# Kernel tuning notes

Hardware: AMD Instinct MI355X
Metric: run time of the kernel (lower is better)

The kernel has to match this reference:

```python
import jax, jax.numpy as jnp
import numpy as np

# Qwen3.5 GatedDeltaNet dims
B, T, HID = 2, 2048, 2048
HK, HV, DK, DV, KW = 16, 32, 128, 128, 4   # k-heads, v-heads, head dims, conv kernel
R = HV // HK                                # GQA repeat factor = 2
KEY_DIM = HK * DK                           # 2048
VAL_DIM = HV * DV                           # 4096
CONV_DIM = 2 * KEY_DIM + VAL_DIM            # 8192
EPS = 1e-6


def setup_inputs() -> dict:
    key = jax.random.key(0)
    ks = jax.random.split(key, 10)
    w = lambda k, shape, s=0.02: (jax.random.normal(k, shape) * s).astype(jnp.float32)
    A = jax.random.uniform(ks[8], (HV,), minval=1e-3, maxval=16.0)
    return {
        "hidden_states": jax.random.normal(ks[0], (B, T, HID), jnp.float32),
        "W_qkv": w(ks[1], (HID, CONV_DIM)),
        "W_z": w(ks[2], (HID, VAL_DIM)),
        "W_b": w(ks[3], (HID, HV)),
        "W_a": w(ks[4], (HID, HV)),
        "conv_w": w(ks[5], (CONV_DIM, KW), 0.5),   # depthwise causal conv taps
        "dt_bias": jnp.ones((HV,), jnp.float32),
        "A_log": jnp.log(A).astype(jnp.float32),
        "norm_weight": jnp.ones((DV,), jnp.float32),
        "W_out": w(ks[9], (VAL_DIM, HID)),
    }


def _forward(hidden_states, W_qkv, W_z, W_b, W_a, conv_w, dt_bias, A_log, norm_weight, W_out):
    x = hidden_states
    # --- projections ---
    qkv = x @ W_qkv                                    # [B,T,CONV_DIM]
    z = x @ W_z                                        # [B,T,VAL_DIM]
    beta = jax.nn.sigmoid(x @ W_b)                     # [B,T,HV]
    alpha = x @ W_a                                    # [B,T,HV]
    g = -jnp.exp(A_log) * jax.nn.softplus(alpha + dt_bias)  # [B,T,HV] (log-decay <= 0)

    # --- fix_query_key_value_ordering: per-k-head interleaved layout ---
    qkv = qkv.reshape(B, T, HK, 2 * DK + R * DV)
    q, k, v = jnp.split(qkv, [DK, 2 * DK], axis=3)
    mixed = jnp.concatenate([q.reshape(B, T, -1), k.reshape(B, T, -1), v.reshape(B, T, -1)], axis=-1)

    # --- causal depthwise short conv (kernel 4) + SiLU ---
    xp = jnp.pad(mixed, ((0, 0), (KW - 1, 0), (0, 0)))
    conv = sum(conv_w[:, i] * xp[:, i:i + T, :] for i in range(KW))
    conv = jax.nn.silu(conv)

    q, k, v = jnp.split(conv, [KEY_DIM, 2 * KEY_DIM], axis=-1)
    q = q.reshape(B, T, HK, DK)
    k = k.reshape(B, T, HK, DK)
    v = v.reshape(B, T, HV, DV)
    gate = z.reshape(B, T, HV, DV)

    # GQA: repeat q,k heads to match v heads
    q = jnp.repeat(q, R, axis=2)                       # [B,T,HV,DK]
    k = jnp.repeat(k, R, axis=2)

    # l2-norm q,k (use_qk_l2norm_in_kernel=True) and default scale 1/sqrt(DK)
    q = q / jnp.sqrt(jnp.sum(q * q, axis=-1, keepdims=True) + 1e-6)
    k = k / jnp.sqrt(jnp.sum(k * k, axis=-1, keepdims=True) + 1e-6)
    q = q * (DK ** -0.5)

    # --- gated delta rule recurrence (scan over time) ---
    # state S: [B,HV,DK,DV];  S_t = a_t*S_{t-1} + k_t (beta_t*(v_t - (a_t*S_{t-1})^T k_t))^T
    def step(S, inp):
        qt, kt, vt, gt, bt = inp                       # [B,HV,DK],[B,HV,DK],[B,HV,DV],[B,HV],[B,HV]
        S = S * jnp.exp(gt)[:, :, None, None]
        kv = jnp.einsum('bhk,bhkv->bhv', kt, S)
        delta = bt[..., None] * (vt - kv)              # [B,HV,DV]
        S = S + kt[..., None] * delta[:, :, None, :]
        o = jnp.einsum('bhk,bhkv->bhv', qt, S)
        return S, o

    tfirst = lambda a: jnp.moveaxis(a, 1, 0)           # [T,B,...]
    S0 = jnp.zeros((B, HV, DK, DV), q.dtype)
    _, o = jax.lax.scan(step, S0, (tfirst(q), tfirst(k), tfirst(v), tfirst(g), tfirst(beta)))
    o = jnp.moveaxis(o, 0, 1)                          # [B,T,HV,DV]

    # --- gated RMSNorm: rmsnorm(o) * silu(gate) * weight ---
    var = jnp.mean(o * o, axis=-1, keepdims=True)
    o = o * jax.lax.rsqrt(var + EPS)
    o = o * jax.nn.silu(gate)
    o = o * norm_weight

    return o.reshape(B, T, VAL_DIM) @ W_out            # [B,T,HID]


def reference(hidden_states, W_qkv, W_z, W_b, W_a, conv_w, dt_bias, A_log, norm_weight, W_out):
    return _forward(hidden_states, W_qkv, W_z, W_b, W_a, conv_w, dt_bias, A_log, norm_weight, W_out)
```

## Files before the change

### kernel.cpp

```cpp
#include <hip/hip_runtime.h>


#define T_LEN 2048
#define MROWS 4096

typedef __bf16 bf16x8 __attribute__((ext_vector_type(8)));
typedef float f32x4 __attribute__((ext_vector_type(4)));

#define MFMA(a, b, c) __builtin_amdgcn_mfma_f32_16x16x32_bf16((a), (b), (c), 0, 0, 0)

__device__ __forceinline__ unsigned short f2bf(float f) {
  unsigned int u = __float_as_uint(f);
  unsigned int r = (u + 0x7fffu + ((u >> 16) & 1u)) >> 16;
  return (unsigned short)r;
}
__device__ __forceinline__ float bf2f(unsigned short u) {
  return __uint_as_float(((unsigned int)u) << 16);
}
__device__ __forceinline__ void gload_lds16(const void* g, void* l) {
  __builtin_amdgcn_global_load_lds(
      (const __attribute__((address_space(1))) unsigned int*)g,
      (__attribute__((address_space(3))) unsigned int*)l, 16, 0, 0);
}

__global__ __launch_bounds__(256) void f32_to_bf16_vec(const float* __restrict__ src,
                                                       unsigned short* __restrict__ dst,
                                                       int n4) {
  int i = blockIdx.x * 256 + threadIdx.x;
  if (i >= n4) return;
  float4 v = ((const float4*)src)[i];
  ushort4 o;
  o.x = f2bf(v.x); o.y = f2bf(v.y); o.z = f2bf(v.z); o.w = f2bf(v.w);
  ((ushort4*)dst)[i] = o;
}

__global__ __launch_bounds__(256) void transpose_f2b(const float* __restrict__ src,
                                                     unsigned short* __restrict__ dst,
                                                     int R, int C) {
  __shared__ float tile[32][33];
  int tx = threadIdx.x & 31, ty = threadIdx.x >> 5;
  int c0 = blockIdx.x * 32, r0 = blockIdx.y * 32;
  #pragma unroll
  for (int i = ty; i < 32; i += 8)
    tile[i][tx] = src[(size_t)(r0 + i) * C + c0 + tx];
  __syncthreads();
  #pragma unroll
  for (int i = ty; i < 32; i += 8)
    dst[(size_t)(c0 + i) * R + r0 + tx] = f2bf(tile[tx][i]);
}

template <int OUTBF>
__global__ __launch_bounds__(512, 2) void gemm8p(const unsigned short* __restrict__ A, int lda,
                                                 const unsigned short* __restrict__ Bt, int ldb,
                                                 void* __restrict__ Cv, int ldc,
                                                 int M, int N, int K) {
  __shared__ unsigned short lds[65536];

  const int mtiles = M >> 8;
  const int nwg = gridDim.x, orig = blockIdx.x;
  const int q = nwg >> 3, r = nwg & 7;
  const int xcd = orig & 7, idx = orig >> 3;
  const int swz = (xcd < r ? xcd * (q + 1) : r * (q + 1) + (xcd - r) * q) + idx;
  const int m0 = (swz % mtiles) * 256;
  const int n0 = (swz / mtiles) * 256;

  const int tid = threadIdx.x, lane = tid & 63, wv = tid >> 6;
  const int wm = wv >> 2, wn = wv & 3;
  const int l15 = lane & 15, l4 = lane >> 4;

  f32x4 acc[8][4];
  #pragma unroll
  for (int i = 0; i < 8; i++)
    #pragma unroll
    for (int j = 0; j < 4; j++) acc[i][j] = f32x4{0.f, 0.f, 0.f, 0.f};

  const int NT = K >> 6;

  auto SHALF = [&](int t, int op, int h) {
    unsigned short* base = lds + (t & 1) * 32768 + op * 16384 + h * 8192;
    const unsigned short* G = op ? Bt : A;
    const int ld = op ? ldb : lda;
    const int r0g = (op ? n0 : m0) + h * 128;
    const int k0 = t << 6;
    #pragma unroll
    for (int is = 0; is < 2; is++) {
      int ow = is * 8192 + wv * 1024;
      int o = ow + lane * 16;
      int row = o >> 7, colB = o & 127;
      int scol = colB ^ ((row & 7) << 4);
      gload_lds16(G + (size_t)(r0g + row) * ld + k0 + (scol >> 1), base + (ow >> 1));
    }
  };

  bf16x8 aF[4][2], bF[2][2];
  auto RD_A = [&](int t, int qm) {
    const unsigned short* base = lds + (t & 1) * 32768 + qm * 8192;
    #pragma unroll
    for (int mi = 0; mi < 4; mi++) {
      int ra = wm * 64 + mi * 16 + l15;
      int sw = (ra & 7) << 4;
      #pragma unroll
      for (int kh = 0; kh < 2; kh++) {
        int colB = kh * 64 + l4 * 16;
        aF[mi][kh] = *(const bf16x8*)(base + ra * 64 + ((colB ^ sw) >> 1));
      }
    }
  };
  auto RD_B = [&](int t, int qn) {
    const unsigned short* base = lds + (t & 1) * 32768 + 16384 + qn * 8192;
    #pragma unroll
    for (int ni = 0; ni < 2; ni++) {
      int rb = wn * 32 + ni * 16 + l15;
      int sw = (rb & 7) << 4;
      #pragma unroll
      for (int kh = 0; kh < 2; kh++) {
        int colB = kh * 64 + l4 * 16;
        bF[ni][kh] = *(const bf16x8*)(base + rb * 64 + ((colB ^ sw) >> 1));
      }
    }
  };
  auto COMPUTE = [&](int qm, int qn) {
    __builtin_amdgcn_s_setprio(1);
    #pragma unroll
    for (int mi = 0; mi < 4; mi++)
      #pragma unroll
      for (int ni = 0; ni < 2; ni++)
        #pragma unroll
        for (int kh = 0; kh < 2; kh++)
          acc[qm * 4 + mi][qn * 2 + ni] =
              MFMA(aF[mi][kh], bF[ni][kh], acc[qm * 4 + mi][qn * 2 + ni]);
    __builtin_amdgcn_s_setprio(0);
  };
  auto SBAR = [&]() {
    __builtin_amdgcn_sched_barrier(0);
    __builtin_amdgcn_s_barrier();
    __builtin_amdgcn_sched_barrier(0);
  };

  SHALF(0, 0, 0); SHALF(0, 1, 0); SHALF(0, 1, 1); SHALF(0, 0, 1);
  asm volatile("s_waitcnt vmcnt(4)" ::: "memory");
  SBAR();

  for (int t = 0; t < NT; t++) {
    const bool lastT = (t + 1 >= NT);
    RD_A(t, 0); RD_B(t, 0);
    if (!lastT) SHALF(t + 1, 0, 0);
    COMPUTE(0, 0);
    if (!lastT) asm volatile("s_waitcnt vmcnt(4)" ::: "memory");
    else        asm volatile("s_waitcnt vmcnt(2)" ::: "memory");
    SBAR();
    RD_B(t, 1);
    if (!lastT) SHALF(t + 1, 1, 0);
    COMPUTE(0, 1);
    if (!lastT) asm volatile("s_waitcnt vmcnt(4)" ::: "memory");
    else        asm volatile("s_waitcnt vmcnt(0)" ::: "memory");
    SBAR();
    RD_A(t, 1);
    if (!lastT) SHALF(t + 1, 1, 1);
    COMPUTE(1, 1);
    RD_B(t, 0);
    if (!lastT) SHALF(t + 1, 0, 1);
    COMPUTE(1, 0);
    if (!lastT) {
      asm volatile("s_waitcnt vmcnt(4)" ::: "memory");
      SBAR();
    }
  }

  #pragma unroll
  for (int i = 0; i < 8; i++) {
    int grow = m0 + (i >> 2) * 128 + wm * 64 + (i & 3) * 16 + l4 * 4;
    #pragma unroll
    for (int j = 0; j < 4; j++) {
      int gcol = n0 + (j >> 1) * 128 + wn * 32 + (j & 1) * 16 + l15;
      if (OUTBF) {
        unsigned short* cp = (unsigned short*)Cv + (size_t)grow * ldc + gcol;
        #pragma unroll
        for (int rr = 0; rr < 4; rr++) cp[(size_t)rr * ldc] = f2bf(acc[i][j][rr]);
      } else {
        float* cp = (float*)Cv + (size_t)grow * ldc + gcol;
        #pragma unroll
        for (int rr = 0; rr < 4; rr++) cp[(size_t)rr * ldc] = acc[i][j][rr];
      }
    }
  }
}

template <int OUTBF, int BN>
__global__ __launch_bounds__(512, 2) void gemm256(const unsigned short* __restrict__ A, int lda,
                                                  const unsigned short* __restrict__ Bt, int ldb,
                                                  void* __restrict__ Cv, int ldc,
                                                  int M, int N, int K) {
  constexpr int BUFSZ = 16384 + BN * 64;
  constexpr int BISS = BN / 64;
  constexpr int IS = 4 + BISS;
  constexpr int WMv = (BN == 256) ? 2 : 4;
  constexpr int MSUB = 256 / (WMv * 16);
  constexpr int MSPAN = 256 / WMv;

  __shared__ unsigned short lds[2 * BUFSZ];

  const int mtiles = M >> 8;
  const int nwg = gridDim.x;
  const int orig = blockIdx.x;
  const int q = nwg >> 3, r = nwg & 7;
  const int xcd = orig & 7, idx = orig >> 3;
  const int swz = (xcd < r ? xcd * (q + 1) : r * (q + 1) + (xcd - r) * q) + idx;
  const int m0 = (swz % mtiles) * 256;
  const int n0 = (swz / mtiles) * BN;

  const int tid = threadIdx.x, lane = tid & 63, wv = tid >> 6;
  const int wm = (BN == 256) ? (wv >> 2) : (wv >> 1);
  const int wn = (BN == 256) ? (wv & 3) : (wv & 1);
  const int l15 = lane & 15, l4 = lane >> 4;

  f32x4 acc[MSUB][4];
  #pragma unroll
  for (int i = 0; i < MSUB; i++)
    #pragma unroll
    for (int j = 0; j < 4; j++) acc[i][j] = f32x4{0.f, 0.f, 0.f, 0.f};

  const int NT = K >> 6;

  auto STAGE = [&](int kt) {
    unsigned short* base = lds + (kt & 1) * BUFSZ;
    const int k0 = kt << 6;
    #pragma unroll
    for (int is = 0; is < 4; is++) {
      int ow = is * 8192 + wv * 1024;
      int o = ow + lane * 16;
      int row = o >> 7, colB = o & 127;
      int scol = colB ^ ((row & 7) << 4);
      gload_lds16(A + (size_t)(m0 + row) * lda + k0 + (scol >> 1), base + (ow >> 1));
    }
    #pragma unroll
    for (int is = 0; is < BISS; is++) {
      int ow = is * 8192 + wv * 1024;
      int o = ow + lane * 16;
      int row = o >> 7, colB = o & 127;
      int scol = colB ^ ((row & 7) << 4);
      gload_lds16(Bt + (size_t)(n0 + row) * ldb + k0 + (scol >> 1), base + 16384 + (ow >> 1));
    }
  };

  STAGE(0);
  if (NT > 1) STAGE(1);
  if constexpr (IS == 8) asm volatile("s_waitcnt vmcnt(8)" ::: "memory");
  else                   asm volatile("s_waitcnt vmcnt(6)" ::: "memory");
  __builtin_amdgcn_sched_barrier(0);
  __builtin_amdgcn_s_barrier();
  __builtin_amdgcn_sched_barrier(0);

  for (int t = 0; t < NT; t++) {
    const unsigned short* Abuf = lds + (t & 1) * BUFSZ;
    const unsigned short* Bbuf = Abuf + 16384;
    bf16x8 bF[4][2];
    #pragma unroll
    for (int n = 0; n < 4; n++) {
      int rb = wn * 64 + n * 16 + l15;
      int sw = (rb & 7) << 4;
      #pragma unroll
      for (int ks = 0; ks < 2; ks++) {
        int colB = (ks * 32 + l4 * 8) * 2;
        bF[n][ks] = *(const bf16x8*)(Bbuf + rb * 64 + ((colB ^ sw) >> 1));
      }
    }
    __builtin_amdgcn_s_setprio(1);
    #pragma unroll
    for (int m = 0; m < MSUB; m++) {
      int ra = wm * MSPAN + m * 16 + l15;
      int sw = (ra & 7) << 4;
      int c0b = l4 * 16;
      bf16x8 a0 = *(const bf16x8*)(Abuf + ra * 64 + ((c0b ^ sw) >> 1));
      bf16x8 a1 = *(const bf16x8*)(Abuf + ra * 64 + (((64 + c0b) ^ sw) >> 1));
      #pragma unroll
      for (int n = 0; n < 4; n++) {
        acc[m][n] = MFMA(a0, bF[n][0], acc[m][n]);
        acc[m][n] = MFMA(a1, bF[n][1], acc[m][n]);
      }
    }
    __builtin_amdgcn_s_setprio(0);
    __builtin_amdgcn_sched_barrier(0);
    __builtin_amdgcn_s_barrier();
    __builtin_amdgcn_sched_barrier(0);
    if (t + 2 < NT) STAGE(t + 2);
    if (t + 1 < NT) {
      if (t + 2 < NT) {
        if constexpr (IS == 8) asm volatile("s_waitcnt vmcnt(8)" ::: "memory");
        else                   asm volatile("s_waitcnt vmcnt(6)" ::: "memory");
      } else {
        asm volatile("s_waitcnt vmcnt(0)" ::: "memory");
      }
      __builtin_amdgcn_sched_barrier(0);
      __builtin_amdgcn_s_barrier();
      __builtin_amdgcn_sched_barrier(0);
    }
  }

  #pragma unroll
  for (int m = 0; m < MSUB; m++) {
    int grow = m0 + wm * MSPAN + m * 16 + l4 * 4;
    #pragma unroll
    for (int n = 0; n < 4; n++) {
      int gcol = n0 + wn * 64 + n * 16 + l15;
      if (OUTBF) {
        unsigned short* cp = (unsigned short*)Cv + (size_t)grow * ldc + gcol;
        #pragma unroll
        for (int rr = 0; rr < 4; rr++) cp[(size_t)rr * ldc] = f2bf(acc[m][n][rr]);
      } else {
        float* cp = (float*)Cv + (size_t)grow * ldc + gcol;
        #pragma unroll
        for (int rr = 0; rr < 4; rr++) cp[(size_t)rr * ldc] = acc[m][n][rr];
      }
    }
  }
}

template <int OUTBF>
__global__ __launch_bounds__(256) void gemm_bf16(const unsigned short* __restrict__ A, int lda,
                                                 const unsigned short* __restrict__ Bt, int ldb,
                                                 void* __restrict__ Cv, int ldc,
                                                 int M, int N, int K) {
  __shared__ unsigned short As[128 * 64];
  __shared__ unsigned short Bs[128 * 64];
  const int tid = threadIdx.x, lane = tid & 63, wv = tid >> 6;
  const int wr = wv >> 1, wc = wv & 1;
  const int m0 = blockIdx.y * 128, n0 = blockIdx.x * 128;
  const int lrow8 = lane >> 3;
  const int lk8 = (lane & 7) * 8;

  f32x4 acc[4][4];
  #pragma unroll
  for (int i = 0; i < 4; i++)
    #pragma unroll
    for (int j = 0; j < 4; j++) acc[i][j] = f32x4{0.f, 0.f, 0.f, 0.f};

  for (int k0 = 0; k0 < K; k0 += 64) {
    #pragma unroll
    for (int j = 0; j < 4; ++j) {
      int chunk = j * 4 + wv;
      int r = chunk * 8 + lrow8;
      gload_lds16(A + (size_t)(m0 + r) * lda + k0 + lk8, (void*)(As + chunk * 512));
      gload_lds16(Bt + (size_t)(n0 + r) * ldb + k0 + lk8, (void*)(Bs + chunk * 512));
    }
    __syncthreads();
    #pragma unroll
    for (int half = 0; half < 2; ++half) {
      int ko = half * 32 + (lane >> 4) * 8;
      bf16x8 af[4], bfr[4];
      #pragma unroll
      for (int i = 0; i < 4; i++) {
        int ra = wr * 64 + i * 16 + (lane & 15);
        af[i] = *(const bf16x8*)(As + ra * 64 + ko);
        int rb = wc * 64 + i * 16 + (lane & 15);
        bfr[i] = *(const bf16x8*)(Bs + rb * 64 + ko);
      }
      #pragma unroll
      for (int i = 0; i < 4; i++)
        #pragma unroll
        for (int j = 0; j < 4; j++)
          acc[i][j] = MFMA(af[i], bfr[j], acc[i][j]);
    }
    __syncthreads();
  }
  int cr4 = (lane >> 4) * 4;
  int cc = lane & 15;
  #pragma unroll
  for (int i = 0; i < 4; i++) {
    int row = m0 + wr * 64 + i * 16 + cr4;
    #pragma unroll
    for (int j = 0; j < 4; j++) {
      int col = n0 + wc * 64 + j * 16 + cc;
      if (OUTBF) {
        unsigned short* cp = (unsigned short*)Cv + (size_t)row * ldc + col;
        #pragma unroll
        for (int r = 0; r < 4; r++) cp[(size_t)r * ldc] = f2bf(acc[i][j][r]);
      } else {
        float* cp = (float*)Cv + (size_t)row * ldc + col;
        #pragma unroll
        for (int r = 0; r < 4; r++) cp[(size_t)r * ldc] = acc[i][j][r];
      }
    }
  }
}

__global__ __launch_bounds__(256) void beta_g_kernel(const unsigned short* __restrict__ ba,
                                                     const float* __restrict__ A_log,
                                                     const float* __restrict__ dt_bias,
                                                     unsigned short* __restrict__ betab,
                                                     float* __restrict__ g) {
  int i = blockIdx.x * 256 + threadIdx.x;
  int row = i >> 5, hv = i & 31;
  float rb = bf2f(ba[(size_t)row * 128 + hv]);
  float ra = bf2f(ba[(size_t)row * 128 + 32 + hv]);
  betab[i] = f2bf(1.f / (1.f + expf(-rb)));
  float xg = ra + dt_bias[hv];
  float sp = (xg > 20.f) ? xg : log1pf(expf(xg));
  g[i] = -expf(A_log[hv]) * sp;
}

__global__ __launch_bounds__(256) void conv_kernel(const unsigned short* __restrict__ qkv,
                                                   const float* __restrict__ conv_w,
                                                   unsigned short* __restrict__ out) {
  const int seg = blockIdx.x, tt = blockIdx.y, b = blockIdx.z;
  const int tid = threadIdx.x;
  const int c0 = seg * 128;
  const bool isq = seg < 16;
  int scb;
  if (isq) scb = seg * 512;
  else if (seg < 32) scb = (seg - 16) * 512 + 128;
  else scb = ((seg - 32) >> 1) * 512 + 256 + ((seg - 32) & 1) * 128;

  __shared__ unsigned short raw[35][136];
  __shared__ float cw[4][132];

  for (int i = tid; i < 512; i += 256) {
    int cl = i >> 2, tap = i & 3;
    cw[tap][cl] = conv_w[(size_t)(c0 + cl) * 4 + tap];
  }
  const int t0 = tt * 32;
  for (int i = tid; i < 560; i += 256) {
    int row = i >> 4, col = (i & 15) * 8;
    int gt = t0 - 3 + row;
    uint4 v = make_uint4(0u, 0u, 0u, 0u);
    if (gt >= 0) v = *(const uint4*)(qkv + (size_t)(b * T_LEN + gt) * 8192 + scb + col);
    *(uint4*)(&raw[row][col]) = v;
  }
  __syncthreads();
  const int s = tid >> 3, dg = tid & 7;
  union RawU { uint4 v[2]; unsigned short h[16]; };
  RawU u[4];
  #pragma unroll
  for (int i = 0; i < 4; i++) {
    const uint4* p = (const uint4*)&raw[s + i][dg * 16];
    u[i].v[0] = p[0]; u[i].v[1] = p[1];
  }
  float vals[16]; float ss = 0.f;
  #pragma unroll
  for (int j = 0; j < 16; j++) {
    float a = 0.f;
    #pragma unroll
    for (int i = 0; i < 4; i++) a = fmaf(cw[i][dg * 16 + j], bf2f(u[i].h[j]), a);
    a = a / (1.f + expf(-a));
    vals[j] = a; ss += a * a;
  }
  if (seg < 32) {
    ss += __shfl_xor(ss, 1); ss += __shfl_xor(ss, 2); ss += __shfl_xor(ss, 4);
    float sc = rsqrtf(ss + 1e-6f);
    if (isq) sc *= 0.08838834764831845f;
    #pragma unroll
    for (int j = 0; j < 16; j++) vals[j] *= sc;
  }
  union { uint4 v[2]; unsigned short h[16]; } ov;
  #pragma unroll
  for (int j = 0; j < 16; j++) ov.h[j] = f2bf(vals[j]);
  unsigned short* op = out + (size_t)(b * T_LEN + t0 + s) * 8192 + c0 + dg * 16;
  *(uint4*)(op) = ov.v[0];
  *(uint4*)(op + 8) = ov.v[1];
}

__global__ __launch_bounds__(256) void prep_kernel(const unsigned short* __restrict__ conv,
                                                   const float* __restrict__ g,
                                                   const unsigned short* __restrict__ betab,
                                                   unsigned short* __restrict__ M1g,
                                                   unsigned short* __restrict__ M2g,
                                                   unsigned char* __restrict__ vecs) {
  const int c = blockIdx.x, bh = blockIdx.y;
  const int b = bh >> 5, hv = bh & 31, hk = hv >> 1;
  const int bhc = bh * 32 + c;
  const int tid = threadIdx.x, lane = tid & 63, wv = tid >> 6;
  const int r0 = b * T_LEN + c * 64;
  const int l15 = lane & 15, l4 = lane >> 4;

  __shared__ unsigned short Kb[128 * 72];
  __shared__ unsigned short QbX[64 * 136];
  __shared__ unsigned short Lbf[64 * 72];
  __shared__ unsigned short Pb[64 * 72];
  __shared__ unsigned short WT[3 * 16 * 40];
  __shared__ float Gs[64], SCs[64], BLs[64];

  unsigned short* Qb = QbX;
  unsigned short* XTb = QbX;
  unsigned short* Xdrow = QbX + 4608;

  if (wv == 0) {
    float gt = g[(size_t)(r0 + lane) * 32 + hv];
    #pragma unroll
    for (int d = 1; d < 64; d <<= 1) {
      float o = __shfl_up(gt, (unsigned)d, 64);
      if (lane >= d) gt += o;
    }
    float GC = __shfl(gt, 63, 64);
    float lam = expf(gt);
    float beta = bf2f(betab[(size_t)(r0 + lane) * 32 + hv]);
    Gs[lane] = gt;
    SCs[lane] = expf(GC - gt);
    BLs[lane] = beta;
    unsigned short* vb16 = (unsigned short*)(vecs + (size_t)bhc * 272);
    vb16[lane] = f2bf(beta * lam);
    vb16[64 + lane] = f2bf(lam);
    if (lane == 0) *(float*)(vecs + (size_t)bhc * 272 + 256) = expf(GC);
  }
  const unsigned short* Kg = conv + (size_t)r0 * 8192 + 2048 + hk * 128;
  const unsigned short* Qg = conv + (size_t)r0 * 8192 + hk * 128;
  for (int u = tid; u < 1024; u += 256) {
    int row = u >> 4, col = (u & 15) * 8;
    *(uint4*)(&Kb[row * 136 + col]) = *(const uint4*)(Kg + (size_t)row * 8192 + col);
    *(uint4*)(&Qb[row * 136 + col]) = *(const uint4*)(Qg + (size_t)row * 8192 + col);
  }
  __syncthreads();

  {
    f32x4 akk[4], aqk[4];
    #pragma unroll
    for (int st = 0; st < 4; st++) { akk[st] = f32x4{0,0,0,0}; aqk[st] = f32x4{0,0,0,0}; }
    int trow = wv * 16 + l15;
    int klo = l4 * 8;
    #pragma unroll
    for (int ks = 0; ks < 4; ks++) {
      int ko = ks * 32 + klo;
      bf16x8 ak = *(const bf16x8*)(&Kb[trow * 136 + ko]);
      bf16x8 aq = *(const bf16x8*)(&Qb[trow * 136 + ko]);
      #pragma unroll
      for (int st = 0; st < 4; st++) {
        bf16x8 bk = *(const bf16x8*)(&Kb[(st * 16 + l15) * 136 + ko]);
        akk[st] = MFMA(ak, bk, akk[st]);
        aqk[st] = MFMA(aq, bk, aqk[st]);
      }
    }
    int orow = wv * 16 + l4 * 4;
    int oc = l15;
    #pragma unroll
    for (int st = 0; st < 4; st++)
      #pragma unroll
      for (int r = 0; r < 4; r++) {
        int t = orow + r, ssv = st * 16 + oc;
        float e = expf(fminf(Gs[t] - Gs[ssv], 0.f));
        Lbf[t * 72 + ssv] = f2bf((ssv < t) ? BLs[t] * e * akk[st][r] : 0.f);
        Pb[t * 72 + ssv] = f2bf((ssv <= t) ? e * aqk[st][r] : 0.f);
      }
  }
  __syncthreads();

  unsigned short ktv[32];
  {
    int dk = tid >> 1, tb = (tid & 1) * 32;
    #pragma unroll
    for (int i = 0; i < 32; i++)
      ktv[i] = f2bf(bf2f(Kb[(tb + i) * 136 + dk]) * SCs[tb + i]);
    for (int u = tid; u < 896; u += 256) {
      *(uint4*)(&QbX[u * 8]) = make_uint4(0u, 0u, 0u, 0u);
    }
    for (int u = tid; u < 240; u += 256) {
      *(uint4*)(&WT[u * 8]) = make_uint4(0u, 0u, 0u, 0u);
    }
  }
  __syncthreads();

  {
    int dk = tid >> 1, tb = (tid & 1) * 32;
    #pragma unroll
    for (int i = 0; i < 32; i++) Kb[dk * 72 + tb + i] = ktv[i];
  }
  {
    const int w16 = wv * 16;
    const int cc = l15;
    float xr[16];
    #pragma unroll
    for (int t = 0; t < 16; t++) {
      float acc = (cc == t) ? 1.f : 0.f;
      union { uint4 v[2]; unsigned short h[16]; } rw;
      const uint4* p = (const uint4*)(&Lbf[(w16 + t) * 72 + w16]);
      rw.v[0] = p[0]; rw.v[1] = p[1];
      #pragma unroll
      for (int s = 0; s < 16; s++) {
        if (s < t) acc = fmaf(-bf2f(rw.h[s]), xr[s], acc);
      }
      xr[t] = acc;
    }
    if (lane < 16) {
      #pragma unroll
      for (int t = 0; t < 16; t++) {
        unsigned short v = f2bf(xr[t]);
        XTb[(w16 + cc) * 72 + w16 + t] = v;
        Xdrow[wv * 640 + t * 40 + cc] = v;
      }
    }
  }
  __syncthreads();

  if (wv < 3) {
    const int j = wv;
    for (int i = j + 1; i < 4; i++) {
      f32x4 w_ = f32x4{0.f, 0.f, 0.f, 0.f};
      #pragma unroll
      for (int ks = 0; ks < 2; ks++) {
        int so = ks * 32 + l4 * 8;
        bf16x8 af = *(const bf16x8*)(&Lbf[(i * 16 + l15) * 72 + so]);
        bf16x8 bfv = *(const bf16x8*)(&XTb[(j * 16 + l15) * 72 + so]);
        w_ = MFMA(af, bfv, w_);
      }
      #pragma unroll
      for (int r = 0; r < 4; r++)
        WT[j * 640 + l15 * 40 + l4 * 4 + r] = f2bf(-w_[r]);
      f32x4 xij = f32x4{0.f, 0.f, 0.f, 0.f};
      {
        bf16x8 af = *(const bf16x8*)(&Xdrow[i * 640 + l15 * 40 + l4 * 8]);
        bf16x8 bfv = *(const bf16x8*)(&WT[j * 640 + l15 * 40 + l4 * 8]);
        xij = MFMA(af, bfv, xij);
      }
      #pragma unroll
      for (int r = 0; r < 4; r++)
        XTb[(j * 16 + l15) * 72 + i * 16 + l4 * 4 + r] = f2bf(xij[r]);
    }
  }
  __syncthreads();

  for (int tt = wv * 12; tt < wv * 12 + 12; tt++) {
    f32x4 acc = f32x4{0, 0, 0, 0};
    const unsigned short* Abase;
    int mrow, jc;
    if (tt < 16) { mrow = (tt >> 2) * 16; jc = (tt & 3) * 16; Abase = Pb + mrow * 72; }
    else { int i2 = tt - 16; mrow = (i2 >> 2) * 16; jc = (i2 & 3) * 16; Abase = Kb + mrow * 72; }
    #pragma unroll
    for (int ks = 0; ks < 2; ks++) {
      int so = ks * 32 + l4 * 8;
      bf16x8 af = *(const bf16x8*)(Abase + l15 * 72 + so);
      bf16x8 bfv = *(const bf16x8*)(&XTb[(jc + l15) * 72 + so]);
      acc = MFMA(af, bfv, acc);
    }
    int ro = mrow + l4 * 4, co = jc + l15;
    if (tt < 16) {
      #pragma unroll
      for (int r = 0; r < 4; r++)
        M1g[(size_t)bhc * 4096 + (ro + r) * 64 + co] = f2bf(acc[r]);
    } else {
      #pragma unroll
      for (int r = 0; r < 4; r++)
        M2g[(size_t)bhc * 8192 + (ro + r) * 64 + co] = f2bf(acc[r]);
    }
  }
}

__global__ __launch_bounds__(512) void seq_kernel(unsigned short* __restrict__ conv,
                                                  const unsigned short* __restrict__ M1g,
                                                  const unsigned short* __restrict__ M2g,
                                                  const unsigned char* __restrict__ vecs,
                                                  const unsigned short* __restrict__ betab) {
  const int bh = blockIdx.x;
  const int b = bh >> 5, hv = bh & 31, hk = hv >> 1;
  const int tid = threadIdx.x, lane = tid & 63, wv = tid >> 6;
  const int l15 = lane & 15, l4 = lane >> 4;

  __shared__ unsigned short Kb[64 * 136], Qb[64 * 136];
  __shared__ unsigned short S0T[128 * 136];
  __shared__ unsigned short rhsT[128 * 72];

  f32x4 S[8];
  #pragma unroll
  for (int i = 0; i < 8; i++) S[i] = f32x4{0.f, 0.f, 0.f, 0.f};

  for (int i = tid; i < 2176; i += 512) *(uint4*)(&S0T[i * 8]) = make_uint4(0u, 0u, 0u, 0u);
  __syncthreads();

  const int trt = (wv >> 1) * 16;
  const int dgb = (wv & 1) * 64;
  const int dkb = wv * 16;

  for (int c = 0; c < 32; c++) {
    const int r0 = b * T_LEN + c * 64;
    const int bhc = bh * 32 + c;
    const unsigned char* vb = vecs + (size_t)bhc * 272;
    const unsigned short* vb16 = (const unsigned short*)vb;
    #pragma unroll
    for (int j = 0; j < 2; j++) {
      int u = j * 512 + tid;
      int row = u >> 4, col = (u & 15) * 8;
      uint4 kv = *(const uint4*)(conv + (size_t)(r0 + row) * 8192 + 2048 + hk * 128 + col);
      uint4 qv = *(const uint4*)(conv + (size_t)(r0 + row) * 8192 + hk * 128 + col);
      *(uint4*)(&Kb[row * 136 + col]) = kv;
      float lam = bf2f(vb16[64 + row]);
      union { uint4 u4; unsigned short h[8]; } qq; qq.u4 = qv;
      #pragma unroll
      for (int e = 0; e < 8; e++) qq.h[e] = f2bf(bf2f(qq.h[e]) * lam);
      *(uint4*)(&Qb[row * 136 + col]) = qq.u4;
    }
    __syncthreads();
    #pragma unroll
    for (int dt = 0; dt < 4; dt++) {
      int dv0 = dgb + dt * 16;
      f32x4 acc = f32x4{0, 0, 0, 0};
      #pragma unroll
      for (int ks = 0; ks < 4; ks++) {
        int ko = ks * 32 + l4 * 8;
        bf16x8 af = *(const bf16x8*)(&Kb[(trt + l15) * 136 + ko]);
        bf16x8 bfv = *(const bf16x8*)(&S0T[(dv0 + l15) * 136 + ko]);
        acc = MFMA(af, bfv, acc);
      }
      #pragma unroll
      for (int r = 0; r < 4; r++) {
        int tl = trt + l4 * 4 + r;
        int t = r0 + tl;
        float beta = bf2f(betab[(size_t)t * 32 + hv]);
        float bl = bf2f(vb16[tl]);
        float vv = bf2f(conv[(size_t)t * 8192 + 4096 + hv * 128 + dv0 + l15]);
        rhsT[(dv0 + l15) * 72 + tl] = f2bf(beta * vv - bl * acc[r]);
      }
    }
    __syncthreads();
    {
      const unsigned short* m1b = M1g + (size_t)bhc * 4096;
      #pragma unroll
      for (int dt = 0; dt < 4; dt++) {
        int dv0 = dgb + dt * 16;
        f32x4 acc = f32x4{0, 0, 0, 0};
        #pragma unroll
        for (int ks = 0; ks < 2; ks++) {
          int so = ks * 32 + l4 * 8;
          union { uint4 u4; bf16x8 h; } af;
          af.u4 = *(const uint4*)(m1b + (trt + l15) * 64 + so);
          bf16x8 bfv = *(const bf16x8*)(&rhsT[(dv0 + l15) * 72 + so]);
          acc = MFMA(af.h, bfv, acc);
        }
        #pragma unroll
        for (int ks = 0; ks < 4; ks++) {
          int ko = ks * 32 + l4 * 8;
          bf16x8 af = *(const bf16x8*)(&Qb[(trt + l15) * 136 + ko]);
          bf16x8 bfv = *(const bf16x8*)(&S0T[(dv0 + l15) * 136 + ko]);
          acc = MFMA(af, bfv, acc);
        }
        #pragma unroll
        for (int r = 0; r < 4; r++) {
          int t = r0 + trt + l4 * 4 + r;
          conv[(size_t)t * 8192 + 4096 + hv * 128 + dv0 + l15] = f2bf(acc[r]);
        }
      }
      float lamC = *(const float*)(vb + 256);
      const unsigned short* m2b = M2g + (size_t)bhc * 8192;
      #pragma unroll
      for (int dvt = 0; dvt < 8; dvt++) {
        f32x4 a = S[dvt];
        a[0] *= lamC; a[1] *= lamC; a[2] *= lamC; a[3] *= lamC;
        #pragma unroll
        for (int ks = 0; ks < 2; ks++) {
          int so = ks * 32 + l4 * 8;
          union { uint4 u4; bf16x8 h; } af;
          af.u4 = *(const uint4*)(m2b + (dkb + l15) * 64 + so);
          bf16x8 bfv = *(const bf16x8*)(&rhsT[(dvt * 16 + l15) * 72 + so]);
          a = MFMA(af.h, bfv, a);
        }
        S[dvt] = a;
      }
    }
    __syncthreads();
    #pragma unroll
    for (int dvt = 0; dvt < 8; dvt++)
      #pragma unroll
      for (int r = 0; r < 4; r++)
        S0T[(dvt * 16 + l15) * 136 + dkb + l4 * 4 + r] = f2bf(S[dvt][r]);
  }
}

__global__ __launch_bounds__(256) void rmsgate_kernel(unsigned short* __restrict__ conv,
                                                      const unsigned short* __restrict__ zg,
                                                      const float* __restrict__ nw) {
  int wid = blockIdx.x * 4 + (threadIdx.x >> 6);
  int lane = threadIdx.x & 63;
  int row = wid >> 5, hv = wid & 31;
  unsigned short* op = conv + (size_t)row * 8192 + 4096 + hv * 128;
  float o0 = bf2f(op[lane]), o1 = bf2f(op[64 + lane]);
  float ss = o0 * o0 + o1 * o1;
  #pragma unroll
  for (int m = 1; m < 64; m <<= 1) ss += __shfl_xor(ss, m);
  float r = rsqrtf(ss * (1.f / 128.f) + 1e-6f);
  const unsigned short* zp = zg + (size_t)row * 4096 + hv * 128;
  float g0 = bf2f(zp[lane]), g1 = bf2f(zp[64 + lane]);
  g0 = g0 / (1.f + expf(-g0));
  g1 = g1 / (1.f + expf(-g1));
  op[lane] = f2bf(o0 * r * g0 * nw[lane]);
  op[64 + lane] = f2bf(o1 * r * g1 * nw[64 + lane]);
}

extern "C" void kernel_launch(void* const* d_in, const int* in_sizes, int n_in,
                              void* d_out, int out_size, void* d_ws, size_t ws_size,
                              hipStream_t stream) {
  (void)in_sizes; (void)n_in; (void)out_size;
  const float* x       = (const float*)d_in[0];
  const float* W_qkv   = (const float*)d_in[1];
  const float* W_z     = (const float*)d_in[2];
  const float* W_b     = (const float*)d_in[3];
  const float* W_a     = (const float*)d_in[4];
  const float* conv_w  = (const float*)d_in[5];
  const float* dt_bias = (const float*)d_in[6];
  const float* A_log   = (const float*)d_in[7];
  const float* nw      = (const float*)d_in[8];
  const float* W_out   = (const float*)d_in[9];
  float* out = (float*)d_out;

  const size_t NEED = 169115648ULL;
  if (ws_size < NEED) return;

  char* ws = (char*)d_ws;
  unsigned short* qkv_bf = (unsigned short*)(ws + 0);
  unsigned short* M1g    = (unsigned short*)(ws + 0);
  unsigned short* M2g    = (unsigned short*)(ws + 16777216);
  unsigned short* WoutT  = (unsigned short*)(ws + 0);
  unsigned short* zg     = (unsigned short*)(ws + 67108864);
  unsigned short* WzT    = (unsigned short*)(ws + 100663296);
  unsigned short* x_bf   = (unsigned short*)(ws + 100663296 + 16777216);
  unsigned short* WqkvT  = (unsigned short*)(ws + 100663296 + 33554432);
  unsigned short* WbaT   = (unsigned short*)(ws + 100663296 + 33554432);
  unsigned short* ba     = (unsigned short*)(ws + 100663296 + 34078720);
  unsigned short* convb  = (unsigned short*)(ws + 100663296);
  unsigned short* betab  = (unsigned short*)(ws + 167772160);
  float* gbuf            = (float*)(ws + 168034304);
  unsigned char* vecs    = (unsigned char*)(ws + 168558592);

  const int M = MROWS;

  f32_to_bf16_vec<<<(M * 2048 / 4) / 256, 256, 0, stream>>>(x, x_bf, M * 2048 / 4);
  transpose_f2b<<<dim3(8192 / 32, 2048 / 32), 256, 0, stream>>>(W_qkv, WqkvT, 2048, 8192);
  transpose_f2b<<<dim3(4096 / 32, 2048 / 32), 256, 0, stream>>>(W_z, WzT, 2048, 4096);

  gemm8p<1><<<512, 512, 0, stream>>>(x_bf, 2048, WqkvT, 2048, qkv_bf, 8192, M, 8192, 2048);

  transpose_f2b<<<dim3(1, 64), 256, 0, stream>>>(W_b, WbaT, 2048, 32);
  transpose_f2b<<<dim3(1, 64), 256, 0, stream>>>(W_a, WbaT + (size_t)32 * 2048, 2048, 32);

  gemm8p<1><<<256, 512, 0, stream>>>(x_bf, 2048, WzT, 2048, zg, 4096, M, 4096, 2048);
  gemm_bf16<1><<<dim3(1, M / 128), 256, 0, stream>>>(x_bf, 2048, WbaT, 2048, ba, 128, M, 128, 2048);

  beta_g_kernel<<<(M * 32) / 256, 256, 0, stream>>>(ba, A_log, dt_bias, betab, gbuf);

  conv_kernel<<<dim3(64, 64, 2), 256, 0, stream>>>(qkv_bf, conv_w, convb);

  prep_kernel<<<dim3(32, 64), 256, 0, stream>>>(convb, gbuf, betab, M1g, M2g, vecs);

  seq_kernel<<<64, 512, 0, stream>>>(convb, M1g, M2g, vecs, betab);

  rmsgate_kernel<<<32768, 256, 0, stream>>>(convb, zg, nw);

  transpose_f2b<<<dim3(2048 / 32, 4096 / 32), 256, 0, stream>>>(W_out, WoutT, 4096, 2048);
  gemm256<0, 128><<<256, 512, 0, stream>>>(convb + 4096, 8192, WoutT, 4096, out, 2048, M, 2048, 4096);
}
```

Before: 628.2 us.

## Fuse gated RMSNorm into sequential scan kernel and merge weight transposes

Moves the gated RMSNorm into the chunked delta-rule kernel. Row sums of squares are reduced across the two wave halves through shared memory, and the normalized, gated output is written directly, which removes the separate rmsgate pass over the output and z buffers. It also merges the four weight transposes into a single launch to cut launch overhead. This adds LDS usage and an extra barrier per chunk to the latency-bound 64-block sequential kernel, which could slow its critical path. WbaT is relocated to the betab region, and that is only safe if the ordering holds.

```diff
diff --git a/kernel.cpp b/kernel.cpp
--- a/kernel.cpp
+++ b/kernel.cpp
@@ -47,6 +47,32 @@
   #pragma unroll
   for (int i = ty; i < 32; i += 8)
     dst[(size_t)(c0 + i) * R + r0 + tx] = f2bf(tile[tx][i]);
+}
+
+__global__ __launch_bounds__(256) void transpose_multi(const float* __restrict__ Wqkv,
+                                                       const float* __restrict__ Wz,
+                                                       const float* __restrict__ Wb,
+                                                       const float* __restrict__ Wa,
+                                                       unsigned short* __restrict__ WqkvT,
+                                                       unsigned short* __restrict__ WzT,
+                                                       unsigned short* __restrict__ WbaT) {
+  int bid = blockIdx.x;
+  const float* src; unsigned short* dst; int C, cx, ry;
+  if (bid < 16384)              { src = Wqkv; dst = WqkvT; C = 8192; cx = bid & 255; ry = bid >> 8; }
+  else if ((bid -= 16384) < 8192) { src = Wz;  dst = WzT;  C = 4096; cx = bid & 127; ry = bid >> 7; }
+  else if ((bid -= 8192) < 64)  { src = Wb; dst = WbaT; C = 32; cx = 0; ry = bid; }
+  else { bid -= 64;               src = Wa; dst = WbaT + (size_t)32 * 2048; C = 32; cx = 0; ry = bid; }
+  const int R = 2048;
+  __shared__ float tile[32][33];
+  int tx = threadIdx.x & 31, ty = threadIdx.x >> 5;
+  int c0 = cx * 32, r0 = ry * 32;
+  #pragma unroll
+  for (int i = ty; i < 32; i += 8)
+    if (c0 + tx < C) tile[i][tx] = src[(size_t)(r0 + i) * C + c0 + tx];
+  __syncthreads();
+  #pragma unroll
+  for (int i = ty; i < 32; i += 8)
+    if (c0 + i < C) dst[(size_t)(c0 + i) * R + r0 + tx] = f2bf(tile[tx][i]);
 }
 
 template <int OUTBF>
@@ -646,7 +672,9 @@
                                                   const unsigned short* __restrict__ M1g,
                                                   const unsigned short* __restrict__ M2g,
                                                   const unsigned char* __restrict__ vecs,
-                                                  const unsigned short* __restrict__ betab) {
+                                                  const unsigned short* __restrict__ betab,
+                                                  const unsigned short* __restrict__ zg,
+                                                  const float* __restrict__ nw) {
   const int bh = blockIdx.x;
   const int b = bh >> 5, hv = bh & 31, hk = hv >> 1;
   const int tid = threadIdx.x, lane = tid & 63, wv = tid >> 6;
@@ -655,12 +683,16 @@
   __shared__ unsigned short Kb[64 * 136], Qb[64 * 136];
   __shared__ unsigned short S0T[128 * 136];
   __shared__ unsigned short rhsT[128 * 72];
+  __shared__ unsigned short zgb[64 * 136];
+  __shared__ float rs[64][2];
+  __shared__ float nws[128];
 
   f32x4 S[8];
   #pragma unroll
   for (int i = 0; i < 8; i++) S[i] = f32x4{0.f, 0.f, 0.f, 0.f};
 
   for (int i = tid; i < 2176; i += 512) *(uint4*)(&S0T[i * 8]) = make_uint4(0u, 0u, 0u, 0u);
+  if (tid < 128) nws[tid] = nw[tid];
   __syncthreads();
 
   const int trt = (wv >> 1) * 16;
@@ -684,6 +716,8 @@
       #pragma unroll
       for (int e = 0; e < 8; e++) qq.h[e] = f2bf(bf2f(qq.h[e]) * lam);
       *(uint4*)(&Qb[row * 136 + col]) = qq.u4;
+      *(uint4*)(&zgb[row * 136 + col]) =
+          *(const uint4*)(zg + (size_t)(r0 + row) * 4096 + hv * 128 + col);
     }
     __syncthreads();
     #pragma unroll
@@ -708,6 +742,7 @@
       }
     }
     __syncthreads();
+    f32x4 accO[4];
     {
       const unsigned short* m1b = M1g + (size_t)bhc * 4096;
       #pragma unroll
@@ -729,11 +764,17 @@
           bf16x8 bfv = *(const bf16x8*)(&S0T[(dv0 + l15) * 136 + ko]);
           acc = MFMA(af, bfv, acc);
         }
-        #pragma unroll
-        for (int r = 0; r < 4; r++) {
-          int t = r0 + trt + l4 * 4 + r;
-          conv[(size_t)t * 8192 + 4096 + hv * 128 + dv0 + l15] = f2bf(acc[r]);
-        }
+        accO[dt] = acc;
+      }
+      #pragma unroll
+      for (int r = 0; r < 4; r++) {
+        float ssr = accO[0][r] * accO[0][r] + accO[1][r] * accO[1][r] +
+                    accO[2][r] * accO[2][r] + accO[3][r] * accO[3][r];
+        ssr += __shfl_xor(ssr, 1);
+        ssr += __shfl_xor(ssr, 2);
+        ssr += __shfl_xor(ssr, 4);
+        ssr += __shfl_xor(ssr, 8);
+        if (l15 == 0) rs[trt + l4 * 4 + r][wv & 1] = ssr;
       }
       float lamC = *(const float*)(vb + 256);
       const unsigned short* m2b = M2g + (size_t)bhc * 8192;
@@ -754,31 +795,26 @@
     }
     __syncthreads();
     #pragma unroll
+    for (int r = 0; r < 4; r++) {
+      int trow = trt + l4 * 4 + r;
+      float rtot = rsqrtf((rs[trow][0] + rs[trow][1]) * 0.0078125f + 1e-6f);
+      int t = r0 + trow;
+      #pragma unroll
+      for (int dt = 0; dt < 4; dt++) {
+        int dv = dgb + dt * 16 + l15;
+        float zf = bf2f(zgb[trow * 136 + dv]);
+        float gate = zf / (1.f + expf(-zf));
+        conv[(size_t)t * 8192 + 4096 + hv * 128 + dv] =
+            f2bf(accO[dt][r] * rtot * gate * nws[dv]);
+      }
+    }
+    #pragma unroll
     for (int dvt = 0; dvt < 8; dvt++)
       #pragma unroll
       for (int r = 0; r < 4; r++)
         S0T[(dvt * 16 + l15) * 136 + dkb + l4 * 4 + r] = f2bf(S[dvt][r]);
-  }
-}
-
-__global__ __launch_bounds__(256) void rmsgate_kernel(unsigned short* __restrict__ conv,
-                                                      const unsigned short* __restrict__ zg,
-                                                      const float* __restrict__ nw) {
-  int wid = blockIdx.x * 4 + (threadIdx.x >> 6);
-  int lane = threadIdx.x & 63;
-  int row = wid >> 5, hv = wid & 31;
-  unsigned short* op = conv + (size_t)row * 8192 + 4096 + hv * 128;
-  float o0 = bf2f(op[lane]), o1 = bf2f(op[64 + lane]);
-  float ss = o0 * o0 + o1 * o1;
-  #pragma unroll
-  for (int m = 1; m < 64; m <<= 1) ss += __shfl_xor(ss, m);
-  float r = rsqrtf(ss * (1.f / 128.f) + 1e-6f);
-  const unsigned short* zp = zg + (size_t)row * 4096 + hv * 128;
-  float g0 = bf2f(zp[lane]), g1 = bf2f(zp[64 + lane]);
-  g0 = g0 / (1.f + expf(-g0));
-  g1 = g1 / (1.f + expf(-g1));
-  op[lane] = f2bf(o0 * r * g0 * nw[lane]);
-  op[64 + lane] = f2bf(o1 * r * g1 * nw[64 + lane]);
+    __syncthreads();
+  }
 }
 
 extern "C" void kernel_launch(void* const* d_in, const int* in_sizes, int n_in,
@@ -809,9 +845,9 @@
   unsigned short* WzT    = (unsigned short*)(ws + 100663296);
   unsigned short* x_bf   = (unsigned short*)(ws + 100663296 + 16777216);
   unsigned short* WqkvT  = (unsigned short*)(ws + 100663296 + 33554432);
-  unsigned short* WbaT   = (unsigned short*)(ws + 100663296 + 33554432);
+  unsigned short* convb  = (unsigned short*)(ws + 100663296);
+  unsigned short* WbaT   = (unsigned short*)(ws + 167772160);
   unsigned short* ba     = (unsigned short*)(ws + 100663296 + 34078720);
-  unsigned short* convb  = (unsigned short*)(ws + 100663296);
   unsigned short* betab  = (unsigned short*)(ws + 167772160);
   float* gbuf            = (float*)(ws + 168034304);
   unsigned char* vecs    = (unsigned char*)(ws + 168558592);
@@ -819,14 +855,9 @@
   const int M = MROWS;
 
   f32_to_bf16_vec<<<(M * 2048 / 4) / 256, 256, 0, stream>>>(x, x_bf, M * 2048 / 4);
-  transpose_f2b<<<dim3(8192 / 32, 2048 / 32), 256, 0, stream>>>(W_qkv, WqkvT, 2048, 8192);
-  transpose_f2b<<<dim3(4096 / 32, 2048 / 32), 256, 0, stream>>>(W_z, WzT, 2048, 4096);
+  transpose_multi<<<24704, 256, 0, stream>>>(W_qkv, W_z, W_b, W_a, WqkvT, WzT, WbaT);
 
   gemm8p<1><<<512, 512, 0, stream>>>(x_bf, 2048, WqkvT, 2048, qkv_bf, 8192, M, 8192, 2048);
-
-  transpose_f2b<<<dim3(1, 64), 256, 0, stream>>>(W_b, WbaT, 2048, 32);
-  transpose_f2b<<<dim3(1, 64), 256, 0, stream>>>(W_a, WbaT + (size_t)32 * 2048, 2048, 32);
-
   gemm8p<1><<<256, 512, 0, stream>>>(x_bf, 2048, WzT, 2048, zg, 4096, M, 4096, 2048);
   gemm_bf16<1><<<dim3(1, M / 128), 256, 0, stream>>>(x_bf, 2048, WbaT, 2048, ba, 128, M, 128, 2048);
 
@@ -836,9 +867,7 @@
 
   prep_kernel<<<dim3(32, 64), 256, 0, stream>>>(convb, gbuf, betab, M1g, M2g, vecs);
 
-  seq_kernel<<<64, 512, 0, stream>>>(convb, M1g, M2g, vecs, betab);
-
-  rmsgate_kernel<<<32768, 256, 0, stream>>>(convb, zg, nw);
+  seq_kernel<<<64, 512, 0, stream>>>(convb, M1g, M2g, vecs, betab, zg, nw);
 
   transpose_f2b<<<dim3(2048 / 32, 4096 / 32), 256, 0, stream>>>(W_out, WoutT, 4096, 2048);
   gemm256<0, 128><<<256, 512, 0, stream>>>(convb + 4096, 8192, WoutT, 4096, out, 2048, M, 2048, 4096);
```

Result: slower. 682.6 us (+8.7%).

## Split recurrent scan across value-dim halves and merge weight transposes

Applied to the files above, without the earlier changes.

The sequential delta-rule kernel now launches two blocks per (batch, head), each owning half of the value dimension of the state. This doubles the parallelism of the latency-bound scan. V and beta are staged in shared memory. The key-side work (K/Q loads, K·S product inputs) is duplicated across the two blocks. The four weight transpose launches are merged into one kernel, which requires relocating the W_b/W_a buffer to a region not aliased by the qkv transpose.

```diff
diff --git a/kernel.cpp b/kernel.cpp
--- a/kernel.cpp
+++ b/kernel.cpp
@@ -47,6 +47,32 @@
   #pragma unroll
   for (int i = ty; i < 32; i += 8)
     dst[(size_t)(c0 + i) * R + r0 + tx] = f2bf(tile[tx][i]);
+}
+
+__global__ __launch_bounds__(256) void transpose_multi(const float* __restrict__ Wqkv,
+                                                       const float* __restrict__ Wz,
+                                                       const float* __restrict__ Wb,
+                                                       const float* __restrict__ Wa,
+                                                       unsigned short* __restrict__ WqkvT,
+                                                       unsigned short* __restrict__ WzT,
+                                                       unsigned short* __restrict__ WbaT) {
+  int bid = blockIdx.x;
+  const float* src; unsigned short* dst; int C, cx, ry;
+  if (bid < 16384)              { src = Wqkv; dst = WqkvT; C = 8192; cx = bid & 255; ry = bid >> 8; }
+  else if ((bid -= 16384) < 8192) { src = Wz;  dst = WzT;  C = 4096; cx = bid & 127; ry = bid >> 7; }
+  else if ((bid -= 8192) < 64)  { src = Wb; dst = WbaT; C = 32; cx = 0; ry = bid; }
+  else { bid -= 64;               src = Wa; dst = WbaT + (size_t)32 * 2048; C = 32; cx = 0; ry = bid; }
+  const int R = 2048;
+  __shared__ float tile[32][33];
+  int tx = threadIdx.x & 31, ty = threadIdx.x >> 5;
+  int c0 = cx * 32, r0 = ry * 32;
+  #pragma unroll
+  for (int i = ty; i < 32; i += 8)
+    if (c0 + tx < C) tile[i][tx] = src[(size_t)(r0 + i) * C + c0 + tx];
+  __syncthreads();
+  #pragma unroll
+  for (int i = ty; i < 32; i += 8)
+    if (c0 + i < C) dst[(size_t)(c0 + i) * R + r0 + tx] = f2bf(tile[tx][i]);
 }
 
 template <int OUTBF>
@@ -647,24 +673,27 @@
                                                   const unsigned short* __restrict__ M2g,
                                                   const unsigned char* __restrict__ vecs,
                                                   const unsigned short* __restrict__ betab) {
-  const int bh = blockIdx.x;
+  const int dvh = blockIdx.x * 64;
+  const int bh = blockIdx.y;
   const int b = bh >> 5, hv = bh & 31, hk = hv >> 1;
   const int tid = threadIdx.x, lane = tid & 63, wv = tid >> 6;
   const int l15 = lane & 15, l4 = lane >> 4;
 
   __shared__ unsigned short Kb[64 * 136], Qb[64 * 136];
-  __shared__ unsigned short S0T[128 * 136];
-  __shared__ unsigned short rhsT[128 * 72];
-
-  f32x4 S[8];
-  #pragma unroll
-  for (int i = 0; i < 8; i++) S[i] = f32x4{0.f, 0.f, 0.f, 0.f};
-
-  for (int i = tid; i < 2176; i += 512) *(uint4*)(&S0T[i * 8]) = make_uint4(0u, 0u, 0u, 0u);
+  __shared__ unsigned short Vb[64 * 72];
+  __shared__ unsigned short S0T[64 * 136];
+  __shared__ unsigned short rhsT[64 * 72];
+  __shared__ unsigned short bts[64];
+
+  f32x4 S[4];
+  #pragma unroll
+  for (int i = 0; i < 4; i++) S[i] = f32x4{0.f, 0.f, 0.f, 0.f};
+
+  for (int i = tid; i < 1088; i += 512) *(uint4*)(&S0T[i * 8]) = make_uint4(0u, 0u, 0u, 0u);
   __syncthreads();
 
   const int trt = (wv >> 1) * 16;
-  const int dgb = (wv & 1) * 64;
+  const int dsb = (wv & 1) * 32;
   const int dkb = wv * 16;
 
   for (int c = 0; c < 32; c++) {
@@ -685,10 +714,16 @@
       for (int e = 0; e < 8; e++) qq.h[e] = f2bf(bf2f(qq.h[e]) * lam);
       *(uint4*)(&Qb[row * 136 + col]) = qq.u4;
     }
+    {
+      int row = tid >> 3, col = (tid & 7) * 8;
+      *(uint4*)(&Vb[row * 72 + col]) =
+          *(const uint4*)(conv + (size_t)(r0 + row) * 8192 + 4096 + hv * 128 + dvh + col);
+      if (tid < 64) bts[tid] = betab[(size_t)(r0 + tid) * 32 + hv];
+    }
     __syncthreads();
     #pragma unroll
-    for (int dt = 0; dt < 4; dt++) {
-      int dv0 = dgb + dt * 16;
+    for (int dt = 0; dt < 2; dt++) {
+      int dv0 = dsb + dt * 16;
       f32x4 acc = f32x4{0, 0, 0, 0};
       #pragma unroll
       for (int ks = 0; ks < 4; ks++) {
@@ -700,10 +735,9 @@
       #pragma unroll
       for (int r = 0; r < 4; r++) {
         int tl = trt + l4 * 4 + r;
-        int t = r0 + tl;
-        float beta = bf2f(betab[(size_t)t * 32 + hv]);
+        float beta = bf2f(bts[tl]);
         float bl = bf2f(vb16[tl]);
-        float vv = bf2f(conv[(size_t)t * 8192 + 4096 + hv * 128 + dv0 + l15]);
+        float vv = bf2f(Vb[tl * 72 + dv0 + l15]);
         rhsT[(dv0 + l15) * 72 + tl] = f2bf(beta * vv - bl * acc[r]);
       }
     }
@@ -711,8 +745,8 @@
     {
       const unsigned short* m1b = M1g + (size_t)bhc * 4096;
       #pragma unroll
-      for (int dt = 0; dt < 4; dt++) {
-        int dv0 = dgb + dt * 16;
+      for (int dt = 0; dt < 2; dt++) {
+        int dv0 = dsb + dt * 16;
         f32x4 acc = f32x4{0, 0, 0, 0};
         #pragma unroll
         for (int ks = 0; ks < 2; ks++) {
@@ -732,13 +766,13 @@
         #pragma unroll
         for (int r = 0; r < 4; r++) {
           int t = r0 + trt + l4 * 4 + r;
-          conv[(size_t)t * 8192 + 4096 + hv * 128 + dv0 + l15] = f2bf(acc[r]);
+          conv[(size_t)t * 8192 + 4096 + hv * 128 + dvh + dv0 + l15] = f2bf(acc[r]);
         }
       }
       float lamC = *(const float*)(vb + 256);
       const unsigned short* m2b = M2g + (size_t)bhc * 8192;
       #pragma unroll
-      for (int dvt = 0; dvt < 8; dvt++) {
+      for (int dvt = 0; dvt < 4; dvt++) {
         f32x4 a = S[dvt];
         a[0] *= lamC; a[1] *= lamC; a[2] *= lamC; a[3] *= lamC;
         #pragma unroll
@@ -754,7 +788,7 @@
     }
     __syncthreads();
     #pragma unroll
-    for (int dvt = 0; dvt < 8; dvt++)
+    for (int dvt = 0; dvt < 4; dvt++)
       #pragma unroll
       for (int r = 0; r < 4; r++)
         S0T[(dvt * 16 + l15) * 136 + dkb + l4 * 4 + r] = f2bf(S[dvt][r]);
@@ -809,9 +843,9 @@
   unsigned short* WzT    = (unsigned short*)(ws + 100663296);
   unsigned short* x_bf   = (unsigned short*)(ws + 100663296 + 16777216);
   unsigned short* WqkvT  = (unsigned short*)(ws + 100663296 + 33554432);
-  unsigned short* WbaT   = (unsigned short*)(ws + 100663296 + 33554432);
+  unsigned short* convb  = (unsigned short*)(ws + 100663296);
+  unsigned short* WbaT   = (unsigned short*)(ws + 167772160);
   unsigned short* ba     = (unsigned short*)(ws + 100663296 + 34078720);
-  unsigned short* convb  = (unsigned short*)(ws + 100663296);
   unsigned short* betab  = (unsigned short*)(ws + 167772160);
   float* gbuf            = (float*)(ws + 168034304);
   unsigned char* vecs    = (unsigned char*)(ws + 168558592);
@@ -819,14 +853,9 @@
   const int M = MROWS;
 
   f32_to_bf16_vec<<<(M * 2048 / 4) / 256, 256, 0, stream>>>(x, x_bf, M * 2048 / 4);
-  transpose_f2b<<<dim3(8192 / 32, 2048 / 32), 256, 0, stream>>>(W_qkv, WqkvT, 2048, 8192);
-  transpose_f2b<<<dim3(4096 / 32, 2048 / 32), 256, 0, stream>>>(W_z, WzT, 2048, 4096);
+  transpose_multi<<<24704, 256, 0, stream>>>(W_qkv, W_z, W_b, W_a, WqkvT, WzT, WbaT);
 
   gemm8p<1><<<512, 512, 0, stream>>>(x_bf, 2048, WqkvT, 2048, qkv_bf, 8192, M, 8192, 2048);
-
-  transpose_f2b<<<dim3(1, 64), 256, 0, stream>>>(W_b, WbaT, 2048, 32);
-  transpose_f2b<<<dim3(1, 64), 256, 0, stream>>>(W_a, WbaT + (size_t)32 * 2048, 2048, 32);
-
   gemm8p<1><<<256, 512, 0, stream>>>(x_bf, 2048, WzT, 2048, zg, 4096, M, 4096, 2048);
   gemm_bf16<1><<<dim3(1, M / 128), 256, 0, stream>>>(x_bf, 2048, WbaT, 2048, ba, 128, M, 128, 2048);
 
@@ -836,7 +865,7 @@
 
   prep_kernel<<<dim3(32, 64), 256, 0, stream>>>(convb, gbuf, betab, M1g, M2g, vecs);
 
-  seq_kernel<<<64, 512, 0, stream>>>(convb, M1g, M2g, vecs, betab);
+  seq_kernel<<<dim3(2, 64), 512, 0, stream>>>(convb, M1g, M2g, vecs, betab);
 
   rmsgate_kernel<<<32768, 256, 0, stream>>>(convb, zg, nw);
 
```

Measured after the change: 602.4 us. 4.1% less time.
